# Optimization experiments

Hardware: AMD Instinct MI355X
Metric: run time of the kernel (lower is better)

Reference implementation:

```python
import jax, jax.numpy as jnp
import numpy as np

N = 100000
F_IN = 128
HID = 256
NUM_CLASSES = 64
E = 1600000


def setup_inputs() -> dict:
    key = jax.random.key(0)
    ks = jax.random.split(key, 10)
    x = jax.random.normal(ks[0], (N, F_IN), dtype=jnp.float32)
    edge_index = jax.random.randint(ks[1], (2, E), 0, N, dtype=jnp.int32)
    edge_weight = jax.random.uniform(ks[2], (E,), dtype=jnp.float32)
    def glorot(k, shape):
        lim = np.sqrt(6.0 / (shape[0] + shape[1]))
        return jax.random.uniform(k, shape, jnp.float32, -lim, lim)
    W0 = glorot(ks[3], (F_IN, HID)); b0 = jnp.zeros((HID,), jnp.float32)
    W1 = glorot(ks[4], (HID, HID)); b1 = jnp.zeros((HID,), jnp.float32)
    W2 = glorot(ks[5], (HID, NUM_CLASSES)); b2 = jnp.zeros((NUM_CLASSES,), jnp.float32)
    return {"x": x, "edge_index": edge_index, "edge_weight": edge_weight,
            "W0": W0, "b0": b0, "W1": W1, "b1": b1, "W2": W2, "b2": b2}


def _gcn_norm(edge_index, edge_weight, n_nodes):
    # renormalization trick: add self-loops (weight 1), D^-1/2 A D^-1/2
    loop = jnp.arange(n_nodes, dtype=edge_index.dtype)
    src = jnp.concatenate([edge_index[0], loop])
    dst = jnp.concatenate([edge_index[1], loop])
    w = jnp.concatenate([edge_weight, jnp.ones((n_nodes,), edge_weight.dtype)])
    deg = jax.ops.segment_sum(w, dst, num_segments=n_nodes)
    d_inv_sqrt = jnp.where(deg > 0, jax.lax.rsqrt(jnp.maximum(deg, 1e-12)), 0.0)
    norm = d_inv_sqrt[src] * w * d_inv_sqrt[dst]
    return src, dst, norm


def _gcn_layer(x, src, dst, norm, W, b, act):
    h = x @ W                                  # [N, d_out] project first (cheap dense)
    msg = h[src] * norm[:, None]               # [E+N, d_out] gather + scale
    out = jax.ops.segment_sum(msg, dst, num_segments=x.shape[0]) + b
    return act(out) if act is not None else out


def reference(x, edge_index, edge_weight, W0, b0, W1, b1, W2, b2):
    n_nodes = x.shape[0]
    src, dst, norm = _gcn_norm(edge_index, edge_weight, n_nodes)
    # dropout is identity at inference (training=None)
    h = _gcn_layer(x, src, dst, norm, W0, b0, jax.nn.relu)
    h = _gcn_layer(h, src, dst, norm, W1, b1, jax.nn.relu)
    h = _gcn_layer(h, src, dst, norm, W2, b2, None)
    return h
```

## Files before the change

kernel.cpp:

```cpp
#include <hip/hip_runtime.h>

#define N_NODES 100000
#define F_IN 128
#define HID 256
#define NCLS 64
#define N_EDGES 1600000

typedef _Float16 f16;
typedef f16 half8 __attribute__((ext_vector_type(8)));
typedef f16 half4 __attribute__((ext_vector_type(4)));
typedef float f32x4 __attribute__((ext_vector_type(4)));
typedef unsigned long long u64;

#define FIXED_SCALE 67108864.0f

__global__ void k_init(unsigned long long* __restrict__ degp, int n) {
    int i = blockIdx.x * 256 + threadIdx.x;
    if (i < n) degp[i] = (unsigned long long)(1u << 26);
}

#define EB   6250
#define XB   12500
#define W0B  128
#define W1B  256
#define W2B  64
__global__ __launch_bounds__(256) void mega1(
        const int* __restrict__ dst, const float* __restrict__ ew,
        unsigned long long* __restrict__ degp, int* __restrict__ seq,
        const float* __restrict__ x, f16* __restrict__ xh,
        const float* __restrict__ W0, f16* __restrict__ Wt0,
        const float* __restrict__ W1, f16* __restrict__ Wt1,
        const float* __restrict__ W2, f16* __restrict__ Wt2) {
    int bid = blockIdx.x;
    int t = threadIdx.x;
    if (bid < EB) {
        int i = bid * 256 + t;
        if (i < N_EDGES) {
            unsigned long long c = (1ULL << 40) |
                (unsigned long long)__float2uint_rn(ew[i] * FIXED_SCALE);
            unsigned long long old = atomicAdd(&degp[dst[i]], c);
            seq[i] = (int)(old >> 40);
        }
    } else if (bid < EB + XB) {
        int i = (bid - EB) * 256 + t;
        if (i < N_NODES * (F_IN / 4)) {
            float4 v = *(const float4*)&x[(size_t)i * 4];
            half4 o;
            o[0] = (f16)v.x; o[1] = (f16)v.y; o[2] = (f16)v.z; o[3] = (f16)v.w;
            *(half4*)&xh[(size_t)i * 4] = o;
        }
    } else if (bid < EB + XB + W0B) {
        int i = (bid - EB - XB) * 256 + t;
        int k = i / HID, d = i % HID;
        Wt0[d * F_IN + k] = (f16)W0[i];
    } else if (bid < EB + XB + W0B + W1B) {
        int i = (bid - EB - XB - W0B) * 256 + t;
        int k = i / HID, d = i % HID;
        Wt1[d * HID + k] = (f16)W1[i];
    } else {
        int i = (bid - EB - XB - W0B - W1B) * 256 + t;
        int k = i / NCLS, d = i % NCLS;
        Wt2[d * HID + k] = (f16)W2[i];
    }
}

__global__ void k_scan1(const unsigned long long* __restrict__ degp,
                        int* __restrict__ cnt, float* __restrict__ dis,
                        float* __restrict__ selfnorm,
                        int* __restrict__ incl, int* __restrict__ bsum, int n) {
    __shared__ int s[256];
    int t = threadIdx.x;
    int i = blockIdx.x * 256 + t;
    int v = 0;
    if (i < n) {
        unsigned long long p = degp[i];
        v = (int)(p >> 40);
        cnt[i] = v;
        float deg = (float)(p & ((1ULL << 40) - 1)) * (1.0f / FIXED_SCALE);
        float d = rsqrtf(deg);
        dis[i] = d;
        selfnorm[i] = d * d;
    }
    s[t] = v;
    __syncthreads();
    #pragma unroll
    for (int off = 1; off < 256; off <<= 1) {
        int x = (t >= off) ? s[t - off] : 0;
        __syncthreads();
        s[t] += x;
        __syncthreads();
    }
    if (i < n) incl[i] = s[t];
    if (t == 255) bsum[blockIdx.x] = s[255];
}

__global__ void k_scan2(const int* __restrict__ bsum, int* __restrict__ boff, int nb) {
    __shared__ int s[512];
    int t = threadIdx.x;
    int v = (t < nb) ? bsum[t] : 0;
    s[t] = v;
    __syncthreads();
    #pragma unroll
    for (int off = 1; off < 512; off <<= 1) {
        int x = (t >= off) ? s[t - off] : 0;
        __syncthreads();
        s[t] += x;
        __syncthreads();
    }
    if (t < nb) boff[t] = s[t] - v;
}

__global__ void k_scan3(int* __restrict__ row, const int* __restrict__ cnt,
                        const int* __restrict__ boff, int n) {
    int i = blockIdx.x * 256 + threadIdx.x;
    if (i < n) row[i] = row[i] - cnt[i] + boff[i >> 8];
}

__global__ void k_place(const int* __restrict__ src, const int* __restrict__ dst,
                        const float* __restrict__ w, const int* __restrict__ seq,
                        const int* __restrict__ row, const float* __restrict__ dis,
                        int2* __restrict__ csr, int e) {
    int i = blockIdx.x * 256 + threadIdx.x;
    if (i < e) {
        int s = src[i], d = dst[i];
        float nw = dis[s] * w[i] * dis[d];
        int pos = row[d] + seq[i];
        csr[pos] = make_int2(s, __float_as_int(nw));
    }
}

template <int K, int DOUT, bool BIAS_RELU>
__global__ __launch_bounds__(256) void gemm_mfma(const f16* __restrict__ in,
                                                 const f16* __restrict__ Wt,
                                                 const float* __restrict__ bias,
                                                 f16* __restrict__ out,
                                                 int nNodes) {
    constexpr int BM = 128, BN = 64, BK = 32;
    constexpr int NB = DOUT / BN;
    constexpr int AP = 40;
    constexpr int CP = 72;
    constexpr int SMEM = (BM * AP + BN * AP) > (BM * CP) ? (BM * AP + BN * AP) : (BM * CP);
    __shared__ f16 smem[SMEM];
    f16* As = smem;
    f16* Bs = smem + BM * AP;

    const int nwg = gridDim.x;
    const int b = blockIdx.x;
    const int q = nwg >> 3, r = nwg & 7, xcd = b & 7;
    const int wk = (xcd < r ? xcd * (q + 1) : r * (q + 1) + (xcd - r) * q) + (b >> 3);
    const int bx = wk / NB, by = wk % NB;

    const int t = threadIdx.x;
    const int w = t >> 6;
    const int lane = t & 63;
    const int quad = lane >> 4;
    const int l16 = lane & 15;
    const int nodeBase = bx * BM;
    const int colBase = by * BN;

    f32x4 acc[2][4] = {};

    for (int k0 = 0; k0 < K; k0 += BK) {
        {
            int koff = (t & 3) * 8;
            #pragma unroll
            for (int p = 0; p < 2; ++p) {
                int r2 = (t >> 2) + p * 64;
                int gn = nodeBase + r2;
                if (gn >= nNodes) gn = nNodes - 1;
                half8 v = *(const half8*)&in[(size_t)gn * K + k0 + koff];
                *(half8*)&As[r2 * AP + koff] = v;
            }
        }
        {
            int koff = (t & 3) * 8;
            int c = t >> 2;
            half8 v = *(const half8*)&Wt[(size_t)(colBase + c) * K + k0 + koff];
            *(half8*)&Bs[c * AP + koff] = v;
        }
        __syncthreads();

        half8 a[2];
        #pragma unroll
        for (int rt = 0; rt < 2; ++rt)
            a[rt] = *(const half8*)&As[(w * 32 + rt * 16 + l16) * AP + quad * 8];
        #pragma unroll
        for (int ct = 0; ct < 4; ++ct) {
            half8 bf = *(const half8*)&Bs[(ct * 16 + l16) * AP + quad * 8];
            acc[0][ct] = __builtin_amdgcn_mfma_f32_16x16x32_f16(a[0], bf, acc[0][ct], 0, 0, 0);
            acc[1][ct] = __builtin_amdgcn_mfma_f32_16x16x32_f16(a[1], bf, acc[1][ct], 0, 0, 0);
        }
        __syncthreads();
    }

    float bv[4];
    #pragma unroll
    for (int ct = 0; ct < 4; ++ct)
        bv[ct] = BIAS_RELU ? bias[colBase + ct * 16 + l16] : 0.0f;

    f16* Cs = smem;
    #pragma unroll
    for (int rt = 0; rt < 2; ++rt)
        #pragma unroll
        for (int ct = 0; ct < 4; ++ct)
            #pragma unroll
            for (int rr2 = 0; rr2 < 4; ++rr2) {
                int rr = w * 32 + rt * 16 + quad * 4 + rr2;
                int cc = ct * 16 + l16;
                float v = acc[rt][ct][rr2];
                if (BIAS_RELU) v = fmaxf(v + bv[ct], 0.0f);
                Cs[rr * CP + cc] = (f16)v;
            }
    __syncthreads();
    #pragma unroll
    for (int p = 0; p < 4; ++p) {
        int rr = (t >> 3) + p * 32;
        int gn = nodeBase + rr;
        int chunk = (t & 7) * 8;
        if (gn < nNodes)
            *(half8*)&out[(size_t)gn * DOUT + colBase + chunk] =
                *(const half8*)&Cs[rr * CP + chunk];
    }
}

template <int DOUT, int TPN, bool HAS_BIAS, bool OUT_F32>
__global__ __launch_bounds__(256) void agg_csr(const f16* __restrict__ h,
                                               const int2* __restrict__ csr,
                                               const int* __restrict__ row,
                                               const int* __restrict__ cnt,
                                               const float* __restrict__ sn,
                                               const float* __restrict__ bias,
                                               void* __restrict__ outv, int nNodes) {
    constexpr int NPB = 256 / TPN;
    int node = blockIdx.x * NPB + threadIdx.x / TPN;
    if (node >= nNodes) return;
    int lane = threadIdx.x % TPN;
    int col = lane * 8;

    float s = sn[node];
    half8 hv = *(const half8*)&h[(size_t)node * DOUT + col];
    float acc[8];
    #pragma unroll
    for (int i = 0; i < 8; ++i)
        acc[i] = s * (float)hv[i] + (HAS_BIAS ? bias[col + i] : 0.0f);

    int e = row[node];
    int end = e + cnt[node];

    for (; e + 3 < end; e += 4) {
        int2 e0 = csr[e], e1 = csr[e + 1], e2 = csr[e + 2], e3 = csr[e + 3];
        float w0 = __int_as_float(e0.y), w1 = __int_as_float(e1.y);
        float w2 = __int_as_float(e2.y), w3 = __int_as_float(e3.y);
        half8 a0 = *(const half8*)&h[(size_t)e0.x * DOUT + col];
        half8 a1 = *(const half8*)&h[(size_t)e1.x * DOUT + col];
        half8 a2 = *(const half8*)&h[(size_t)e2.x * DOUT + col];
        half8 a3 = *(const half8*)&h[(size_t)e3.x * DOUT + col];
        #pragma unroll
        for (int i = 0; i < 8; ++i)
            acc[i] += w0 * (float)a0[i] + w1 * (float)a1[i]
                    + w2 * (float)a2[i] + w3 * (float)a3[i];
    }
    for (; e + 1 < end; e += 2) {
        int2 e0 = csr[e], e1 = csr[e + 1];
        float w0 = __int_as_float(e0.y), w1 = __int_as_float(e1.y);
        half8 a0 = *(const half8*)&h[(size_t)e0.x * DOUT + col];
        half8 a1 = *(const half8*)&h[(size_t)e1.x * DOUT + col];
        #pragma unroll
        for (int i = 0; i < 8; ++i) acc[i] += w0 * (float)a0[i] + w1 * (float)a1[i];
    }
    if (e < end) {
        int2 e0 = csr[e];
        float w0 = __int_as_float(e0.y);
        half8 a0 = *(const half8*)&h[(size_t)e0.x * DOUT + col];
        #pragma unroll
        for (int i = 0; i < 8; ++i) acc[i] += w0 * (float)a0[i];
    }

    if (OUT_F32) {
        float* out = (float*)outv;
        float4 r0 = make_float4(acc[0], acc[1], acc[2], acc[3]);
        float4 r1 = make_float4(acc[4], acc[5], acc[6], acc[7]);
        *(float4*)&out[(size_t)node * DOUT + col] = r0;
        *(float4*)&out[(size_t)node * DOUT + col + 4] = r1;
    } else {
        f16* out = (f16*)outv;
        half8 o;
        #pragma unroll
        for (int i = 0; i < 8; ++i) o[i] = (f16)acc[i];
        *(half8*)&out[(size_t)node * DOUT + col] = o;
    }
}

extern "C" void kernel_launch(void* const* d_in, const int* in_sizes, int n_in,
                              void* d_out, int out_size, void* d_ws, size_t ws_size,
                              hipStream_t stream) {
    const float* x  = (const float*)d_in[0];
    const int*   ei = (const int*)d_in[1];
    const float* ew = (const float*)d_in[2];
    const float* W0 = (const float*)d_in[3];
    const float* b0 = (const float*)d_in[4];
    const float* W1 = (const float*)d_in[5];
    const float* b1 = (const float*)d_in[6];
    const float* W2 = (const float*)d_in[7];
    const float* b2 = (const float*)d_in[8];
    const int* src = ei;
    const int* dst = ei + N_EDGES;
    float* outp = (float*)d_out;

    char* ws = (char*)d_ws;
    unsigned long long* degp = (unsigned long long*)ws;  ws += N_NODES * 8;
    int2*  csr      = (int2*)ws;   ws += (size_t)N_EDGES * 8;
    int*   seq      = (int*)ws;    ws += (size_t)N_EDGES * 4;
    float* dis      = (float*)ws;  ws += N_NODES * 4;
    float* selfnorm = (float*)ws;  ws += N_NODES * 4;
    int*   cnt      = (int*)ws;    ws += N_NODES * 4;
    int*   row      = (int*)ws;    ws += N_NODES * 4;
    int*   bsum     = (int*)ws;    ws += 512 * 4;
    int*   boff     = (int*)ws;    ws += 512 * 4;
    f16*   xh       = (f16*)ws;    ws += (size_t)N_NODES * F_IN * 2;
    f16*   Wt0      = (f16*)ws;    ws += F_IN * HID * 2;
    f16*   Wt1      = (f16*)ws;    ws += HID * HID * 2;
    f16*   Wt2      = (f16*)ws;    ws += HID * NCLS * 2;
    f16*   bufA     = (f16*)ws;    ws += (size_t)N_NODES * HID * 2;
    f16*   bufB     = (f16*)ws;    ws += (size_t)N_NODES * HID * 2;

    const int nb = (N_NODES + 255) / 256;
    const int eb = (N_EDGES + 255) / 256;

    k_init<<<nb, 256, 0, stream>>>(degp, N_NODES);
    mega1<<<EB + XB + W0B + W1B + W2B, 256, 0, stream>>>(
        dst, ew, degp, seq, x, xh, W0, Wt0, W1, Wt1, W2, Wt2);
    k_scan1<<<nb, 256, 0, stream>>>(degp, cnt, dis, selfnorm, row, bsum, N_NODES);
    k_scan2<<<1, 512, 0, stream>>>(bsum, boff, nb);
    k_scan3<<<nb, 256, 0, stream>>>(row, cnt, boff, N_NODES);
    k_place<<<eb, 256, 0, stream>>>(src, dst, ew, seq, row, dis, csr, N_EDGES);

    const int gX = (N_NODES + 127) / 128;

    agg_csr<F_IN, 16, false, false><<<(N_NODES + 15) / 16, 256, 0, stream>>>(
        xh, csr, row, cnt, selfnorm, nullptr, bufA, N_NODES);
    gemm_mfma<F_IN, HID, true><<<gX * (HID / 64), 256, 0, stream>>>(bufA, Wt0, b0, bufB, N_NODES);

    agg_csr<HID, 32, false, false><<<(N_NODES + 7) / 8, 256, 0, stream>>>(
        bufB, csr, row, cnt, selfnorm, nullptr, bufA, N_NODES);
    gemm_mfma<HID, HID, true><<<gX * (HID / 64), 256, 0, stream>>>(bufA, Wt1, b1, bufB, N_NODES);

    gemm_mfma<HID, NCLS, false><<<gX * (NCLS / 64), 256, 0, stream>>>(bufB, Wt2, nullptr, bufA, N_NODES);
    agg_csr<NCLS, 8, true, true><<<(N_NODES + 31) / 32, 256, 0, stream>>>(
        bufA, csr, row, cnt, selfnorm, b2, outp, N_NODES);
}
```

Measured before the change: 519.3 us.

## Drop scan3 kernel, fold row offsets into consumers, split layer-2 aggregation

Removes the k_scan3 pass by computing each row offset on the fly (inclusive count minus count plus block offset) inside k_place and agg_csr. It also drops the 4-way unrolled edge loop in agg_csr, keeping only the 2-way loop, and splits the HID aggregation into two launches over node halves. The aim is to save one kernel launch and one pass over the row array. In exchange, every consumer does a few extra index loads, the aggregation has less memory-level parallelism per thread, and there is one more launch.

New measurement: 541.1 us. +4.2%, slower.

```diff
diff --git a/kernel.cpp b/kernel.cpp
--- a/kernel.cpp
+++ b/kernel.cpp
@@ -110,21 +110,16 @@
     if (t < nb) boff[t] = s[t] - v;
 }
 
-__global__ void k_scan3(int* __restrict__ row, const int* __restrict__ cnt,
-                        const int* __restrict__ boff, int n) {
-    int i = blockIdx.x * 256 + threadIdx.x;
-    if (i < n) row[i] = row[i] - cnt[i] + boff[i >> 8];
-}
-
 __global__ void k_place(const int* __restrict__ src, const int* __restrict__ dst,
                         const float* __restrict__ w, const int* __restrict__ seq,
-                        const int* __restrict__ row, const float* __restrict__ dis,
+                        const int* __restrict__ incl, const int* __restrict__ cnt,
+                        const int* __restrict__ boff, const float* __restrict__ dis,
                         int2* __restrict__ csr, int e) {
     int i = blockIdx.x * 256 + threadIdx.x;
     if (i < e) {
         int s = src[i], d = dst[i];
         float nw = dis[s] * w[i] * dis[d];
-        int pos = row[d] + seq[i];
+        int pos = incl[d] - cnt[d] + boff[d >> 8] + seq[i];
         csr[pos] = make_int2(s, __float_as_int(nw));
     }
 }
@@ -226,14 +221,16 @@
 template <int DOUT, int TPN, bool HAS_BIAS, bool OUT_F32>
 __global__ __launch_bounds__(256) void agg_csr(const f16* __restrict__ h,
                                                const int2* __restrict__ csr,
-                                               const int* __restrict__ row,
+                                               const int* __restrict__ incl,
                                                const int* __restrict__ cnt,
+                                               const int* __restrict__ boff,
                                                const float* __restrict__ sn,
                                                const float* __restrict__ bias,
-                                               void* __restrict__ outv, int nNodes) {
+                                               void* __restrict__ outv,
+                                               int nodeBase, int nodeEnd) {
     constexpr int NPB = 256 / TPN;
-    int node = blockIdx.x * NPB + threadIdx.x / TPN;
-    if (node >= nNodes) return;
+    int node = nodeBase + blockIdx.x * NPB + threadIdx.x / TPN;
+    if (node >= nodeEnd) return;
     int lane = threadIdx.x % TPN;
     int col = lane * 8;
 
@@ -244,22 +241,10 @@
     for (int i = 0; i < 8; ++i)
         acc[i] = s * (float)hv[i] + (HAS_BIAS ? bias[col + i] : 0.0f);
 
-    int e = row[node];
-    int end = e + cnt[node];
-
-    for (; e + 3 < end; e += 4) {
-        int2 e0 = csr[e], e1 = csr[e + 1], e2 = csr[e + 2], e3 = csr[e + 3];
-        float w0 = __int_as_float(e0.y), w1 = __int_as_float(e1.y);
-        float w2 = __int_as_float(e2.y), w3 = __int_as_float(e3.y);
-        half8 a0 = *(const half8*)&h[(size_t)e0.x * DOUT + col];
-        half8 a1 = *(const half8*)&h[(size_t)e1.x * DOUT + col];
-        half8 a2 = *(const half8*)&h[(size_t)e2.x * DOUT + col];
-        half8 a3 = *(const half8*)&h[(size_t)e3.x * DOUT + col];
-        #pragma unroll
-        for (int i = 0; i < 8; ++i)
-            acc[i] += w0 * (float)a0[i] + w1 * (float)a1[i]
-                    + w2 * (float)a2[i] + w3 * (float)a3[i];
-    }
+    int c = cnt[node];
+    int end = incl[node] + boff[node >> 8];
+    int e = end - c;
+
     for (; e + 1 < end; e += 2) {
         int2 e0 = csr[e], e1 = csr[e + 1];
         float w0 = __int_as_float(e0.y), w1 = __int_as_float(e1.y);
@@ -314,7 +299,7 @@
     float* dis      = (float*)ws;  ws += N_NODES * 4;
     float* selfnorm = (float*)ws;  ws += N_NODES * 4;
     int*   cnt      = (int*)ws;    ws += N_NODES * 4;
-    int*   row      = (int*)ws;    ws += N_NODES * 4;
+    int*   incl     = (int*)ws;    ws += N_NODES * 4;
     int*   bsum     = (int*)ws;    ws += 512 * 4;
     int*   boff     = (int*)ws;    ws += 512 * 4;
     f16*   xh       = (f16*)ws;    ws += (size_t)N_NODES * F_IN * 2;
@@ -330,22 +315,24 @@
     k_init<<<nb, 256, 0, stream>>>(degp, N_NODES);
     mega1<<<EB + XB + W0B + W1B + W2B, 256, 0, stream>>>(
         dst, ew, degp, seq, x, xh, W0, Wt0, W1, Wt1, W2, Wt2);
-    k_scan1<<<nb, 256, 0, stream>>>(degp, cnt, dis, selfnorm, row, bsum, N_NODES);
+    k_scan1<<<nb, 256, 0, stream>>>(degp, cnt, dis, selfnorm, incl, bsum, N_NODES);
     k_scan2<<<1, 512, 0, stream>>>(bsum, boff, nb);
-    k_scan3<<<nb, 256, 0, stream>>>(row, cnt, boff, N_NODES);
-    k_place<<<eb, 256, 0, stream>>>(src, dst, ew, seq, row, dis, csr, N_EDGES);
+    k_place<<<eb, 256, 0, stream>>>(src, dst, ew, seq, incl, cnt, boff, dis, csr, N_EDGES);
 
     const int gX = (N_NODES + 127) / 128;
+    const int HALF = N_NODES / 2;
 
     agg_csr<F_IN, 16, false, false><<<(N_NODES + 15) / 16, 256, 0, stream>>>(
-        xh, csr, row, cnt, selfnorm, nullptr, bufA, N_NODES);
+        xh, csr, incl, cnt, boff, selfnorm, nullptr, bufA, 0, N_NODES);
     gemm_mfma<F_IN, HID, true><<<gX * (HID / 64), 256, 0, stream>>>(bufA, Wt0, b0, bufB, N_NODES);
 
-    agg_csr<HID, 32, false, false><<<(N_NODES + 7) / 8, 256, 0, stream>>>(
-        bufB, csr, row, cnt, selfnorm, nullptr, bufA, N_NODES);
+    agg_csr<HID, 32, false, false><<<HALF / 8, 256, 0, stream>>>(
+        bufB, csr, incl, cnt, boff, selfnorm, nullptr, bufA, 0, HALF);
+    agg_csr<HID, 32, false, false><<<(N_NODES - HALF + 7) / 8, 256, 0, stream>>>(
+        bufB, csr, incl, cnt, boff, selfnorm, nullptr, bufA, HALF, N_NODES);
     gemm_mfma<HID, HID, true><<<gX * (HID / 64), 256, 0, stream>>>(bufA, Wt1, b1, bufB, N_NODES);
 
     gemm_mfma<HID, NCLS, false><<<gX * (NCLS / 64), 256, 0, stream>>>(bufB, Wt2, nullptr, bufA, N_NODES);
     agg_csr<NCLS, 8, true, true><<<(N_NODES + 31) / 32, 256, 0, stream>>>(
-        bufA, csr, row, cnt, selfnorm, b2, outp, N_NODES);
-}
+        bufA, csr, incl, cnt, boff, selfnorm, b2, outp, 0, N_NODES);
+}
```
